# Kernel tuning notes

Measured on AMD Instinct MI355X. Metric: run time of the kernel, lower is better.

Reference implementation:

```python
import jax, jax.numpy as jnp
import numpy as np

EPS = 1e-6
NUM_SPECIAL = 4
NUM_HEADS = 16


def _rms_norm(x, w, eps=EPS):
    # x: [..., d], normalize over last dim
    var = jnp.mean(jnp.square(x), axis=-1, keepdims=True)
    return x * jax.lax.rsqrt(var + eps) * w


def _rotate_half(x):
    d = x.shape[-1] // 2
    return jnp.concatenate([-x[..., d:], x[..., :d]], axis=-1)


def _apply_rotary(q, k, cos, sin):
    # q,k: [B,H,N,hd]; cos,sin: [N,hd] -> broadcast [1,1,N,hd]
    cos = cos[None, None, :, :]
    sin = sin[None, None, :, :]
    q_out = q * cos + _rotate_half(q) * sin
    k_out = k * cos + _rotate_half(k) * sin
    return q_out, k_out


def _make_2d_mask(seq_len, num_special, window):
    # special tokens attend / are attended fully; patches use 2D local box
    patch_len = seq_len - num_special
    gs = int(round(patch_len ** 0.5))
    idx = jnp.arange(seq_len)
    special = idx < num_special
    p = idx - num_special
    row = p // gs
    col = p % gs
    special_case = special[:, None] | special[None, :]
    swa = (jnp.abs(row[:, None] - row[None, :]) <= window) & (
        jnp.abs(col[:, None] - col[None, :]) <= window)
    return special_case | swa  # [N, N] bool


def setup_inputs() -> dict:
    key = jax.random.key(0)
    ks = jax.random.split(key, 7)
    B, N, C = 4, 1028, 1024
    hd = C // NUM_HEADS
    return {
        "hidden_states": jax.random.normal(ks[0], (B, N, C), dtype=jnp.float32),
        "cos": jax.random.uniform(ks[1], (N, hd), dtype=jnp.float32),
        "sin": jax.random.uniform(ks[2], (N, hd), dtype=jnp.float32),
        "qkv_w": jax.random.normal(ks[3], (3 * C, C), dtype=jnp.float32) * (C ** -0.5),
        "out_w": jax.random.normal(ks[4], (C, C), dtype=jnp.float32) * (C ** -0.5),
        "norm_q_w": jnp.ones((hd,), dtype=jnp.float32),
        "norm_k_w": jnp.ones((hd,), dtype=jnp.float32),
        "sliding_window": 2,
    }


def reference(hidden_states, cos, sin, qkv_w, out_w, norm_q_w, norm_k_w, sliding_window):
    B, N, C = hidden_states.shape
    H = NUM_HEADS
    hd = C // H

    # fused QKV projection (nn.Linear: x @ W^T)
    qkv = jnp.einsum('bnc,dc->bnd', hidden_states, qkv_w)
    qkv = qkv.reshape(B, N, 3, H, hd).transpose(2, 0, 3, 1, 4)  # [3,B,H,N,hd]
    q, k, v = qkv[0], qkv[1], qkv[2]

    # per-head-dim RMSNorm on q and k
    q = _rms_norm(q, norm_q_w)
    k = _rms_norm(k, norm_k_w)

    # RoPE
    q, k = _apply_rotary(q, k, cos, sin)

    # 2D sliding-window + special-token mask
    mask = _make_2d_mask(N, NUM_SPECIAL, sliding_window)  # [N,N]

    scale = 1.0 / jnp.sqrt(jnp.asarray(hd, dtype=q.dtype))
    scores = jnp.einsum('bhqd,bhkd->bhqk', q, k) * scale
    neg = jnp.asarray(jnp.finfo(scores.dtype).min, dtype=scores.dtype)
    scores = jnp.where(mask[None, None, :, :], scores, neg)
    probs = jax.nn.softmax(scores, axis=-1)
    attn = jnp.einsum('bhqk,bhkd->bhqd', probs, v)  # [B,H,N,hd]

    attn = attn.transpose(0, 2, 1, 3).reshape(B, N, C)
    return jnp.einsum('bnc,dc->bnd', attn, out_w)
```

## Files before the change

kernel.cpp:

```cpp
#include <hip/hip_runtime.h>
#include <hip/hip_bf16.h>
#include <stdint.h>

typedef __bf16 bf16;
typedef __attribute__((ext_vector_type(8))) __bf16 bf16x8;
typedef __attribute__((ext_vector_type(4))) __bf16 bf16x4;
typedef __attribute__((ext_vector_type(4))) float f32x4;

#define NSEQ 1028
#define CDIM 1024
#define NHEADS 16
#define HD 64
#define BHN 64
#define NPAD 1088
#define M_REAL 4112
#define MTILES 33

static __device__ __forceinline__ void async_copy16(bf16* lds, const bf16* g) {
  __builtin_amdgcn_global_load_lds(
      (const __attribute__((address_space(1))) uint32_t*)g,
      (__attribute__((address_space(3))) uint32_t*)lds, 16, 0, 0);
}

__global__ __launch_bounds__(256) void cast3_kernel(
    const float* __restrict__ s0, bf16* __restrict__ d0, long n0,
    const float* __restrict__ s1, bf16* __restrict__ d1, long n1,
    const float* __restrict__ s2, bf16* __restrict__ d2, long n2) {
  long total = n0 + n1 + n2;
  long t = (long)blockIdx.x * 256 + threadIdx.x;
  long stride = (long)gridDim.x * 256;
  for (long j = t * 4; j < total; j += stride * 4) {
    const float* s; bf16* d; long jj = j;
    if (jj < n0) { s = s0; d = d0; }
    else if (jj < n0 + n1) { s = s1; d = d1; jj -= n0; }
    else { s = s2; d = d2; jj -= n0 + n1; }
    float4 v = *(const float4*)(s + jj);
    bf16x4 o;
    o[0] = (bf16)v.x; o[1] = (bf16)v.y; o[2] = (bf16)v.z; o[3] = (bf16)v.w;
    *(bf16x4*)(d + jj) = o;
  }
}

template <int EPI, int NSTRIP>
__global__ __launch_bounds__(256, 4) void gemm_bf16_kernel(
    const bf16* __restrict__ A, const bf16* __restrict__ Bm,
    bf16* __restrict__ q_bf, bf16* __restrict__ k_bf, bf16* __restrict__ v_raw,
    float* __restrict__ outF,
    const float* __restrict__ cosb, const float* __restrict__ sinb,
    const float* __restrict__ nqw, const float* __restrict__ nkw) {
  constexpr int K = CDIM;
  constexpr int N = NSTRIP * 8 * 128;
  __shared__ __attribute__((aligned(16))) bf16 As[2][128 * 32];
  __shared__ __attribute__((aligned(16))) bf16 Bs[2][128 * 32];
  const int tid = threadIdx.x;
  const int lane = tid & 63;
  const int wid = tid >> 6;
  const int wr = wid >> 1, wc = wid & 1;
  const int l15 = lane & 15, l4 = lane >> 4;

  const int xcd = blockIdx.x & 7;
  const int pos = blockIdx.x >> 3;
  const int nloc = pos % NSTRIP;
  const int mi = pos / NSTRIP;
  const int n0 = (xcd * NSTRIP + nloc) << 7;
  const int m0 = (mi < MTILES - 1) ? (mi << 7) : (M_REAL - 128);

  f32x4 acc[4][4] = {};

  size_t a_base[2], b_base[2];
#pragma unroll
  for (int s = 0; s < 2; s++) {
    int c = tid + s * 256;
    int u = c ^ ((c >> 3) & 7);
    int row = u >> 2, ch = u & 3;
    a_base[s] = (size_t)(m0 + row) * K + (ch << 3);
    b_base[s] = (size_t)(n0 + row) * K + (ch << 3);
  }

#define STAGE(bufi, ktof)                                         \
  {                                                               \
    _Pragma("unroll")                                             \
    for (int s = 0; s < 2; s++) {                                 \
      int c = tid + s * 256;                                      \
      async_copy16(&As[bufi][c * 8], A + a_base[s] + (ktof));     \
      async_copy16(&Bs[bufi][c * 8], Bm + b_base[s] + (ktof));    \
    }                                                             \
  }

  const int nt = K >> 5;
  STAGE(0, 0);

  for (int t = 0; t < nt; ++t) {
    if (t + 1 < nt) {
      STAGE((t + 1) & 1, (t + 1) << 5);
      asm volatile("s_waitcnt vmcnt(4)" ::: "memory");
    } else {
      asm volatile("s_waitcnt vmcnt(0)" ::: "memory");
    }
    __builtin_amdgcn_s_barrier();

    const int cur = t & 1;
    bf16x8 af[4], bfr[4];
#pragma unroll
    for (int i = 0; i < 4; i++) {
      int u = ((wr * 64 + i * 16 + l15) << 2) | l4;
      af[i] = *(const bf16x8*)&As[cur][(u ^ ((u >> 3) & 7)) << 3];
    }
#pragma unroll
    for (int j = 0; j < 4; j++) {
      int u = ((wc * 64 + j * 16 + l15) << 2) | l4;
      bfr[j] = *(const bf16x8*)&Bs[cur][(u ^ ((u >> 3) & 7)) << 3];
    }

#pragma unroll
    for (int i = 0; i < 4; i++)
#pragma unroll
      for (int j = 0; j < 4; j++)
        acc[i][j] = __builtin_amdgcn_mfma_f32_16x16x32_bf16(af[i], bfr[j], acc[i][j], 0, 0, 0);

    asm volatile("s_waitcnt lgkmcnt(0)" ::: "memory");
    __builtin_amdgcn_s_barrier();
  }
#undef STAGE

  if (EPI == 0) {
    const int d_base = n0 + wc * 64;
    const int tsel = d_base >> 10;
    const int hh = (d_base & 1023) >> 6;
    if (tsel == 2) {
#pragma unroll
      for (int i = 0; i < 4; i++)
#pragma unroll
        for (int r = 0; r < 4; r++) {
          int m = m0 + wr * 64 + i * 16 + l4 * 4 + r;
          int b = m / NSEQ, n = m % NSEQ;
          size_t rb = ((size_t)(b * NHEADS + hh) * NSEQ + n) * HD;
#pragma unroll
          for (int j = 0; j < 4; j++)
            v_raw[rb + j * 16 + l15] = (bf16)acc[i][j][r];
        }
    } else {
      const float* wn = (tsel == 0) ? nqw : nkw;
      bf16* dst = (tsel == 0) ? q_bf : k_bf;
      float wv[4];
#pragma unroll
      for (int j = 0; j < 4; j++) wv[j] = wn[j * 16 + l15];
#pragma unroll
      for (int i = 0; i < 4; i++)
#pragma unroll
        for (int r = 0; r < 4; r++) {
          int m = m0 + wr * 64 + i * 16 + l4 * 4 + r;
          float ss = 0.0f;
#pragma unroll
          for (int j = 0; j < 4; j++) { float x = acc[i][j][r]; ss += x * x; }
          ss += __shfl_xor(ss, 1);
          ss += __shfl_xor(ss, 2);
          ss += __shfl_xor(ss, 4);
          ss += __shfl_xor(ss, 8);
          float rms = rsqrtf(ss * (1.0f / HD) + 1e-6f);
          int b = m / NSEQ, n = m % NSEQ;
          float qn[4];
#pragma unroll
          for (int j = 0; j < 4; j++) qn[j] = acc[i][j][r] * rms * wv[j];
          size_t rb = ((size_t)(b * NHEADS + hh) * NPAD + n) * HD;
#pragma unroll
          for (int j = 0; j < 4; j++) {
            float c = cosb[n * HD + j * 16 + l15];
            float s = sinb[n * HD + j * 16 + l15];
            float rot = (j < 2) ? -qn[j + 2] : qn[j - 2];
            dst[rb + j * 16 + l15] = (bf16)(qn[j] * c + rot * s);
          }
        }
    }
  } else {
#pragma unroll
    for (int i = 0; i < 4; i++)
#pragma unroll
      for (int j = 0; j < 4; j++) {
        int d = n0 + wc * 64 + j * 16 + l15;
        int mrow = m0 + wr * 64 + i * 16 + l4 * 4;
#pragma unroll
        for (int r = 0; r < 4; r++) {
          int m = mrow + r;
          outF[(size_t)m * N + d] = acc[i][j][r];
        }
      }
  }
}

__global__ __launch_bounds__(256) void v_transpose_kernel(const bf16* __restrict__ v_raw,
                                                          bf16* __restrict__ vT) {
  __shared__ bf16 tile[64][65];
  int bh = blockIdx.y, c = blockIdx.x;
  int tid = threadIdx.x;
#pragma unroll
  for (int jj = 0; jj < 16; jj++) {
    int idx = tid + jj * 256;
    int i = idx >> 6, e = idx & 63;
    int n = (c == 0) ? i : (64 * c - 60 + i);
    bool ok = (c == 0) ? (i < 4) : (n < NSEQ);
    tile[i][e] = ok ? v_raw[((size_t)bh * NSEQ + n) * HD + e] : (bf16)0.0f;
  }
  __syncthreads();
#pragma unroll
  for (int jj = 0; jj < 16; jj++) {
    int idx = tid + jj * 256;
    int e = idx >> 6, i = idx & 63;
    vT[((size_t)bh * HD + e) * NPAD + 64 * c + i] = tile[i][e];
  }
}

__global__ __launch_bounds__(256) void attn_kernel(
    const bf16* __restrict__ Q, const bf16* __restrict__ Kb, const bf16* __restrict__ Vt,
    bf16* __restrict__ att, const int* __restrict__ winp) {
  __shared__ __attribute__((aligned(16))) bf16 P_s[4][16][72];
  __shared__ float o_s[4][4][64];
  __shared__ float ml_s[4][2][16];
  const int bh = blockIdx.y, qt = blockIdx.x;
  const int W = winp[0];
  const int tid = threadIdx.x, w = tid >> 6, lane = tid & 63;
  const int l15 = lane & 15, l4 = lane >> 4;
  const size_t qkbase = (size_t)bh * NPAD * HD;
  const size_t vtb = (size_t)bh * HD * NPAD;
  const bool is_spec = (qt == 16);

  const int qrow0 = is_spec ? 0 : (4 + qt * 64 + w * 16);
  bf16x8 aq0 = *(const bf16x8*)&Q[qkbase + (size_t)(qrow0 + l15) * HD + l4 * 8];
  bf16x8 aq1 = *(const bf16x8*)&Q[qkbase + (size_t)(qrow0 + l15) * HD + 32 + l4 * 8];

  float mrow[4], lrow[4];
  f32x4 o[4] = {};
#pragma unroll
  for (int r = 0; r < 4; r++) { mrow[r] = -1e30f; lrow[r] = 0.0f; }

  int p0, pstep, pmax, toff;
  if (is_spec) {
    p0 = w; pstep = 4; pmax = 16; toff = -1;
  } else {
    int ta = ((2 * qt - W + 64) >> 1) - 32;
    int tb = (2 * qt + 1 + W) >> 1;
    ta = ta < 0 ? 0 : ta;
    tb = tb > 15 ? 15 : tb;
    p0 = 0; pstep = 1; pmax = tb - ta + 1; toff = ta - 1;
  }

  for (int p = p0; p <= pmax; p += pstep) {
    const bool sp = (p == 0);
    const int tau = toff + p;
    const int krow0 = sp ? 0 : (4 + tau * 64);
    const int vcol0 = sp ? 0 : (64 + tau * 64);

    f32x4 sacc[4] = {};
#pragma unroll
    for (int kf = 0; kf < 4; kf++) {
      const bf16* kp = &Kb[qkbase + (size_t)(krow0 + kf * 16 + l15) * HD];
      bf16x8 b0 = *(const bf16x8*)(kp + l4 * 8);
      bf16x8 b1 = *(const bf16x8*)(kp + 32 + l4 * 8);
      sacc[kf] = __builtin_amdgcn_mfma_f32_16x16x32_bf16(aq0, b0, sacc[kf], 0, 0, 0);
      sacc[kf] = __builtin_amdgcn_mfma_f32_16x16x32_bf16(aq1, b1, sacc[kf], 0, 0, 0);
    }

    float pvv[4][4];
#pragma unroll
    for (int kf = 0; kf < 4; kf++)
#pragma unroll
      for (int r = 0; r < 4; r++) {
        float s = sacc[kf][r] * 0.125f;
        bool valid;
        if (sp) {
          valid = (kf == 0) && (l15 < 4);
        } else if (is_spec) {
          valid = true;
        } else {
          int p_k = tau * 64 + kf * 16 + l15;
          int p_q = qt * 64 + w * 16 + l4 * 4 + r;
          int dr = (p_q >> 5) - (p_k >> 5); dr = dr < 0 ? -dr : dr;
          int dc = (p_q & 31) - (p_k & 31); dc = dc < 0 ? -dc : dc;
          valid = (dr <= W) && (dc <= W);
        }
        pvv[kf][r] = valid ? s : -1e30f;
      }

#pragma unroll
    for (int r = 0; r < 4; r++) {
      float mx = fmaxf(fmaxf(pvv[0][r], pvv[1][r]), fmaxf(pvv[2][r], pvv[3][r]));
#pragma unroll
      for (int mm = 1; mm < 16; mm <<= 1) mx = fmaxf(mx, __shfl_xor(mx, mm));
      float mnew = fmaxf(mrow[r], mx);
      float scale = __expf(mrow[r] - mnew);
      float rs = 0.0f;
#pragma unroll
      for (int kf = 0; kf < 4; kf++) {
        float pp = __expf(pvv[kf][r] - mnew);
        pvv[kf][r] = pp;
        rs += pp;
      }
#pragma unroll
      for (int mm = 1; mm < 16; mm <<= 1) rs += __shfl_xor(rs, mm);
      lrow[r] = lrow[r] * scale + rs;
      mrow[r] = mnew;
#pragma unroll
      for (int f = 0; f < 4; f++) o[f][r] *= scale;
    }

#pragma unroll
    for (int kf = 0; kf < 4; kf++)
#pragma unroll
      for (int r = 0; r < 4; r++)
        P_s[w][l4 * 4 + r][kf * 16 + l15] = (bf16)pvv[kf][r];

    bf16x8 pa0 = *(const bf16x8*)&P_s[w][l15][l4 * 8];
    bf16x8 pa1 = *(const bf16x8*)&P_s[w][l15][32 + l4 * 8];
#pragma unroll
    for (int f = 0; f < 4; f++) {
      const bf16* vp = &Vt[vtb + (size_t)(f * 16 + l15) * NPAD + vcol0];
      bf16x8 v0 = *(const bf16x8*)(vp + l4 * 8);
      bf16x8 v1 = *(const bf16x8*)(vp + 32 + l4 * 8);
      o[f] = __builtin_amdgcn_mfma_f32_16x16x32_bf16(pa0, v0, o[f], 0, 0, 0);
      o[f] = __builtin_amdgcn_mfma_f32_16x16x32_bf16(pa1, v1, o[f], 0, 0, 0);
    }
  }

  const int b = bh >> 4, h = bh & 15;
  if (!is_spec) {
#pragma unroll
    for (int f = 0; f < 4; f++)
#pragma unroll
      for (int r = 0; r < 4; r++) {
        int n = qrow0 + l4 * 4 + r;
        att[((size_t)(b * NSEQ + n)) * CDIM + h * HD + f * 16 + l15] =
            (bf16)(o[f][r] / lrow[r]);
      }
  } else {
    if (l4 == 0) {
#pragma unroll
      for (int f = 0; f < 4; f++)
#pragma unroll
        for (int r = 0; r < 4; r++) o_s[w][r][f * 16 + l15] = o[f][r];
      if (l15 == 0)
#pragma unroll
        for (int r = 0; r < 4; r++) { ml_s[w][0][r] = mrow[r]; ml_s[w][1][r] = lrow[r]; }
    }
    __syncthreads();
    int row = tid >> 6, dim = tid & 63;
    float M = -1e30f;
#pragma unroll
    for (int ww = 0; ww < 4; ww++) M = fmaxf(M, ml_s[ww][0][row]);
    float L = 0.0f, val = 0.0f;
#pragma unroll
    for (int ww = 0; ww < 4; ww++) {
      float e = __expf(ml_s[ww][0][row] - M);
      L += e * ml_s[ww][1][row];
      val += e * o_s[ww][row][dim];
    }
    att[((size_t)(b * NSEQ + row)) * CDIM + h * HD + dim] = (bf16)(val / L);
  }
}

extern "C" void kernel_launch(void* const* d_in, const int* in_sizes, int n_in,
                              void* d_out, int out_size, void* d_ws, size_t ws_size,
                              hipStream_t stream) {
  const float* hidden = (const float*)d_in[0];
  const float* cosb = (const float*)d_in[1];
  const float* sinb = (const float*)d_in[2];
  const float* qkv_w = (const float*)d_in[3];
  const float* out_w = (const float*)d_in[4];
  const float* norm_q_w = (const float*)d_in[5];
  const float* norm_k_w = (const float*)d_in[6];
  const int* win = (const int*)d_in[7];
  float* out = (float*)d_out;

  char* ws = (char*)d_ws;
  size_t off = 0;
  auto alloc = [&](size_t bytes) {
    char* p = ws + off;
    off += (bytes + 255) & ~(size_t)255;
    return p;
  };
  bf16* A_bf  = (bf16*)alloc((size_t)M_REAL * CDIM * 2);
  bf16* W1    = (bf16*)alloc((size_t)3 * CDIM * CDIM * 2);
  bf16* W2    = (bf16*)alloc((size_t)CDIM * CDIM * 2);
  bf16* v_raw = (bf16*)alloc((size_t)BHN * NSEQ * HD * 2);
  bf16* q_bf  = (bf16*)alloc((size_t)BHN * NPAD * HD * 2);
  bf16* k_bf  = (bf16*)alloc((size_t)BHN * NPAD * HD * 2);
  bf16* vT    = (bf16*)alloc((size_t)BHN * HD * NPAD * 2);
  bf16* att   = (bf16*)alloc((size_t)M_REAL * CDIM * 2);
  (void)ws_size; (void)in_sizes; (void)n_in; (void)out_size;

  cast3_kernel<<<2048, 256, 0, stream>>>(
      hidden, A_bf, (long)M_REAL * CDIM,
      qkv_w, W1, (long)3 * CDIM * CDIM,
      out_w, W2, (long)CDIM * CDIM);

  gemm_bf16_kernel<0, 3><<<792, 256, 0, stream>>>(
      A_bf, W1, q_bf, k_bf, v_raw, nullptr, cosb, sinb, norm_q_w, norm_k_w);
  v_transpose_kernel<<<dim3(17, 64), 256, 0, stream>>>(v_raw, vT);
  attn_kernel<<<dim3(17, 64), 256, 0, stream>>>(q_bf, k_bf, vT, att, win);
  gemm_bf16_kernel<1, 1><<<264, 256, 0, stream>>>(
      att, W2, nullptr, nullptr, nullptr, out, nullptr, nullptr, nullptr, nullptr);
}
```

Before: 130.6 us.

## Load GEMM B operand directly to registers and shrink output GEMM N-tile

The GEMM no longer stages the weight (B) tile through LDS. Each wave reads its B fragments straight from global memory into registers every k-step, which halves the LDS footprint, and the occupancy hint rises from 4 to 6 blocks. The output projection now uses a 64-wide N tile with twice as many blocks, giving more parallelism. In exchange, the B loads are not prefetched, so global/L2 latency is exposed inside each k iteration, and weights are re-read per wave without LDS sharing.

```diff
diff --git a/kernel.cpp b/kernel.cpp
--- a/kernel.cpp
+++ b/kernel.cpp
@@ -41,17 +41,18 @@
   }
 }
 
-template <int EPI, int NSTRIP>
-__global__ __launch_bounds__(256, 4) void gemm_bf16_kernel(
+template <int EPI, int NSTRIP, int BN>
+__global__ __launch_bounds__(256, 6) void gemm_bf16_kernel(
     const bf16* __restrict__ A, const bf16* __restrict__ Bm,
     bf16* __restrict__ q_bf, bf16* __restrict__ k_bf, bf16* __restrict__ v_raw,
     float* __restrict__ outF,
     const float* __restrict__ cosb, const float* __restrict__ sinb,
     const float* __restrict__ nqw, const float* __restrict__ nkw) {
   constexpr int K = CDIM;
-  constexpr int N = NSTRIP * 8 * 128;
+  constexpr int N = NSTRIP * 8 * BN;
+  constexpr int HN = BN / 2;
+  constexpr int NJ = BN / 32;
   __shared__ __attribute__((aligned(16))) bf16 As[2][128 * 32];
-  __shared__ __attribute__((aligned(16))) bf16 Bs[2][128 * 32];
   const int tid = threadIdx.x;
   const int lane = tid & 63;
   const int wid = tid >> 6;
@@ -62,60 +63,58 @@
   const int pos = blockIdx.x >> 3;
   const int nloc = pos % NSTRIP;
   const int mi = pos / NSTRIP;
-  const int n0 = (xcd * NSTRIP + nloc) << 7;
+  const int n0 = (xcd * NSTRIP + nloc) * BN;
   const int m0 = (mi < MTILES - 1) ? (mi << 7) : (M_REAL - 128);
 
-  f32x4 acc[4][4] = {};
-
-  size_t a_base[2], b_base[2];
+  f32x4 acc[4][NJ] = {};
+
+  size_t a_base[2];
 #pragma unroll
   for (int s = 0; s < 2; s++) {
     int c = tid + s * 256;
     int u = c ^ ((c >> 3) & 7);
-    int row = u >> 2, ch = u & 3;
-    a_base[s] = (size_t)(m0 + row) * K + (ch << 3);
-    b_base[s] = (size_t)(n0 + row) * K + (ch << 3);
-  }
+    a_base[s] = (size_t)(m0 + (u >> 2)) * K + ((u & 3) << 3);
+  }
+
+  const size_t b_uni = (size_t)(n0 + wc * HN) * K;
+  const int b_lane = l15 * K + l4 * 8;
 
 #define STAGE(bufi, ktof)                                         \
   {                                                               \
     _Pragma("unroll")                                             \
-    for (int s = 0; s < 2; s++) {                                 \
-      int c = tid + s * 256;                                      \
-      async_copy16(&As[bufi][c * 8], A + a_base[s] + (ktof));     \
-      async_copy16(&Bs[bufi][c * 8], Bm + b_base[s] + (ktof));    \
-    }                                                             \
+    for (int s = 0; s < 2; s++)                                   \
+      async_copy16(&As[bufi][(tid + s * 256) * 8], A + a_base[s] + (ktof)); \
   }
 
   const int nt = K >> 5;
   STAGE(0, 0);
 
   for (int t = 0; t < nt; ++t) {
+    bf16x8 bfr[NJ];
+#pragma unroll
+    for (int j = 0; j < NJ; j++)
+      bfr[j] = *(const bf16x8*)(Bm + b_uni + (size_t)j * 16 * K + b_lane + (t << 5));
+
     if (t + 1 < nt) {
       STAGE((t + 1) & 1, (t + 1) << 5);
-      asm volatile("s_waitcnt vmcnt(4)" ::: "memory");
+      asm volatile("s_waitcnt vmcnt(2)" ::: "memory");
     } else {
       asm volatile("s_waitcnt vmcnt(0)" ::: "memory");
     }
     __builtin_amdgcn_s_barrier();
 
     const int cur = t & 1;
-    bf16x8 af[4], bfr[4];
+    bf16x8 af[4];
 #pragma unroll
     for (int i = 0; i < 4; i++) {
       int u = ((wr * 64 + i * 16 + l15) << 2) | l4;
       af[i] = *(const bf16x8*)&As[cur][(u ^ ((u >> 3) & 7)) << 3];
     }
-#pragma unroll
-    for (int j = 0; j < 4; j++) {
-      int u = ((wc * 64 + j * 16 + l15) << 2) | l4;
-      bfr[j] = *(const bf16x8*)&Bs[cur][(u ^ ((u >> 3) & 7)) << 3];
-    }
 
 #pragma unroll
     for (int i = 0; i < 4; i++)
 #pragma unroll
-      for (int j = 0; j < 4; j++)
+      for (int j = 0; j < NJ; j++)
         acc[i][j] = __builtin_amdgcn_mfma_f32_16x16x32_bf16(af[i], bfr[j], acc[i][j], 0, 0, 0);
 
     asm volatile("s_waitcnt lgkmcnt(0)" ::: "memory");
@@ -136,15 +135,15 @@
           int b = m / NSEQ, n = m % NSEQ;
           size_t rb = ((size_t)(b * NHEADS + hh) * NSEQ + n) * HD;
 #pragma unroll
-          for (int j = 0; j < 4; j++)
+          for (int j = 0; j < NJ; j++)
             v_raw[rb + j * 16 + l15] = (bf16)acc[i][j][r];
         }
     } else {
       const float* wn = (tsel == 0) ? nqw : nkw;
       bf16* dst = (tsel == 0) ? q_bf : k_bf;
-      float wv[4];
-#pragma unroll
-      for (int j = 0; j < 4; j++) wv[j] = wn[j * 16 + l15];
+      float wv[NJ];
+#pragma unroll
+      for (int j = 0; j < NJ; j++) wv[j] = wn[j * 16 + l15];
 #pragma unroll
       for (int i = 0; i < 4; i++)
 #pragma unroll
@@ -152,19 +151,19 @@
           int m = m0 + wr * 64 + i * 16 + l4 * 4 + r;
           float ss = 0.0f;
 #pragma unroll
-          for (int j = 0; j < 4; j++) { float x = acc[i][j][r]; ss += x * x; }
+          for (int j = 0; j < NJ; j++) { float x = acc[i][j][r]; ss += x * x; }
           ss += __shfl_xor(ss, 1);
           ss += __shfl_xor(ss, 2);
           ss += __shfl_xor(ss, 4);
           ss += __shfl_xor(ss, 8);
           float rms = rsqrtf(ss * (1.0f / HD) + 1e-6f);
           int b = m / NSEQ, n = m % NSEQ;
-          float qn[4];
-#pragma unroll
-          for (int j = 0; j < 4; j++) qn[j] = acc[i][j][r] * rms * wv[j];
+          float qn[NJ];
+#pragma unroll
+          for (int j = 0; j < NJ; j++) qn[j] = acc[i][j][r] * rms * wv[j];
           size_t rb = ((size_t)(b * NHEADS + hh) * NPAD + n) * HD;
 #pragma unroll
-          for (int j = 0; j < 4; j++) {
+          for (int j = 0; j < NJ; j++) {
             float c = cosb[n * HD + j * 16 + l15];
             float s = sinb[n * HD + j * 16 + l15];
             float rot = (j < 2) ? -qn[j + 2] : qn[j - 2];
@@ -176,8 +175,8 @@
 #pragma unroll
     for (int i = 0; i < 4; i++)
 #pragma unroll
-      for (int j = 0; j < 4; j++) {
-        int d = n0 + wc * 64 + j * 16 + l15;
+      for (int j = 0; j < NJ; j++) {
+        int d = n0 + wc * HN + j * 16 + l15;
         int mrow = m0 + wr * 64 + i * 16 + l4 * 4;
 #pragma unroll
         for (int r = 0; r < 4; r++) {
@@ -392,10 +391,10 @@
       qkv_w, W1, (long)3 * CDIM * CDIM,
       out_w, W2, (long)CDIM * CDIM);
 
-  gemm_bf16_kernel<0, 3><<<792, 256, 0, stream>>>(
+  gemm_bf16_kernel<0, 3, 128><<<792, 256, 0, stream>>>(
       A_bf, W1, q_bf, k_bf, v_raw, nullptr, cosb, sinb, norm_q_w, norm_k_w);
   v_transpose_kernel<<<dim3(17, 64), 256, 0, stream>>>(v_raw, vT);
   attn_kernel<<<dim3(17, 64), 256, 0, stream>>>(q_bf, k_bf, vT, att, win);
-  gemm_bf16_kernel<1, 1><<<264, 256, 0, stream>>>(
+  gemm_bf16_kernel<1, 2, 64><<<528, 256, 0, stream>>>(
       att, W2, nullptr, nullptr, nullptr, out, nullptr, nullptr, nullptr, nullptr);
 }
```

Measured after the change: 328.1 us. +151.2%, slower.

## Split output projection GEMM into intra-block split-K with 64-wide tiles

Applied to the files above, without the earlier changes.

The output projection now uses a dedicated kernel with 128x64 tiles and 528 blocks instead of 264 128x128 blocks. Inside each block, two wave pairs each handle half of K and reduce their partial sums through LDS before the fp32 store. This is meant to fill the GPU's compute units better, since the old launch had too few blocks. It also adds s_setprio around MFMA sections in the GEMM and attention kernels to favour matrix issue. The cost is extra LDS traffic for the reduction and more loads per output.

```diff
diff --git a/kernel.cpp b/kernel.cpp
--- a/kernel.cpp
+++ b/kernel.cpp
@@ -41,15 +41,13 @@
   }
 }
 
-template <int EPI, int NSTRIP>
-__global__ __launch_bounds__(256, 4) void gemm_bf16_kernel(
+__global__ __launch_bounds__(256, 4) void gemm_qkv_kernel(
     const bf16* __restrict__ A, const bf16* __restrict__ Bm,
     bf16* __restrict__ q_bf, bf16* __restrict__ k_bf, bf16* __restrict__ v_raw,
-    float* __restrict__ outF,
     const float* __restrict__ cosb, const float* __restrict__ sinb,
     const float* __restrict__ nqw, const float* __restrict__ nkw) {
   constexpr int K = CDIM;
-  constexpr int N = NSTRIP * 8 * 128;
+  constexpr int NSTRIP = 3;
   __shared__ __attribute__((aligned(16))) bf16 As[2][128 * 32];
   __shared__ __attribute__((aligned(16))) bf16 Bs[2][128 * 32];
   const int tid = threadIdx.x;
@@ -72,19 +70,17 @@
   for (int s = 0; s < 2; s++) {
     int c = tid + s * 256;
     int u = c ^ ((c >> 3) & 7);
-    int row = u >> 2, ch = u & 3;
-    a_base[s] = (size_t)(m0 + row) * K + (ch << 3);
-    b_base[s] = (size_t)(n0 + row) * K + (ch << 3);
-  }
-
-#define STAGE(bufi, ktof)                                         \
-  {                                                               \
-    _Pragma("unroll")                                             \
-    for (int s = 0; s < 2; s++) {                                 \
-      int c = tid + s * 256;                                      \
-      async_copy16(&As[bufi][c * 8], A + a_base[s] + (ktof));     \
-      async_copy16(&Bs[bufi][c * 8], Bm + b_base[s] + (ktof));    \
-    }                                                             \
+    a_base[s] = (size_t)(m0 + (u >> 2)) * K + ((u & 3) << 3);
+    b_base[s] = (size_t)(n0 + (u >> 2)) * K + ((u & 3) << 3);
+  }
+
+#define STAGE(bufi, ktof)                                                   \
+  {                                                                         \
+    _Pragma("unroll")                                                       \
+    for (int s = 0; s < 2; s++) {                                           \
+      async_copy16(&As[bufi][(tid + s * 256) * 8], A + a_base[s] + (ktof)); \
+      async_copy16(&Bs[bufi][(tid + s * 256) * 8], Bm + b_base[s] + (ktof));\
+    }                                                                       \
   }
 
   const int nt = K >> 5;
@@ -123,68 +119,174 @@
   }
 #undef STAGE
 
-  if (EPI == 0) {
-    const int d_base = n0 + wc * 64;
-    const int tsel = d_base >> 10;
-    const int hh = (d_base & 1023) >> 6;
-    if (tsel == 2) {
-#pragma unroll
-      for (int i = 0; i < 4; i++)
-#pragma unroll
-        for (int r = 0; r < 4; r++) {
-          int m = m0 + wr * 64 + i * 16 + l4 * 4 + r;
-          int b = m / NSEQ, n = m % NSEQ;
-          size_t rb = ((size_t)(b * NHEADS + hh) * NSEQ + n) * HD;
-#pragma unroll
-          for (int j = 0; j < 4; j++)
-            v_raw[rb + j * 16 + l15] = (bf16)acc[i][j][r];
-        }
-    } else {
-      const float* wn = (tsel == 0) ? nqw : nkw;
-      bf16* dst = (tsel == 0) ? q_bf : k_bf;
-      float wv[4];
-#pragma unroll
-      for (int j = 0; j < 4; j++) wv[j] = wn[j * 16 + l15];
-#pragma unroll
-      for (int i = 0; i < 4; i++)
-#pragma unroll
-        for (int r = 0; r < 4; r++) {
-          int m = m0 + wr * 64 + i * 16 + l4 * 4 + r;
-          float ss = 0.0f;
-#pragma unroll
-          for (int j = 0; j < 4; j++) { float x = acc[i][j][r]; ss += x * x; }
-          ss += __shfl_xor(ss, 1);
-          ss += __shfl_xor(ss, 2);
-          ss += __shfl_xor(ss, 4);
-          ss += __shfl_xor(ss, 8);
-          float rms = rsqrtf(ss * (1.0f / HD) + 1e-6f);
-          int b = m / NSEQ, n = m % NSEQ;
-          float qn[4];
-#pragma unroll
-          for (int j = 0; j < 4; j++) qn[j] = acc[i][j][r] * rms * wv[j];
-          size_t rb = ((size_t)(b * NHEADS + hh) * NPAD + n) * HD;
-#pragma unroll
-          for (int j = 0; j < 4; j++) {
-            float c = cosb[n * HD + j * 16 + l15];
-            float s = sinb[n * HD + j * 16 + l15];
-            float rot = (j < 2) ? -qn[j + 2] : qn[j - 2];
-            dst[rb + j * 16 + l15] = (bf16)(qn[j] * c + rot * s);
-          }
-        }
-    }
+  const int d_base = n0 + wc * 64;
+  const int tsel = d_base >> 10;
+  const int hh = (d_base & 1023) >> 6;
+  if (tsel == 2) {
+#pragma unroll
+    for (int i = 0; i < 4; i++)
+#pragma unroll
+      for (int r = 0; r < 4; r++) {
+        int m = m0 + wr * 64 + i * 16 + l4 * 4 + r;
+        int b = m / NSEQ, n = m % NSEQ;
+        size_t rb = ((size_t)(b * NHEADS + hh) * NSEQ + n) * HD;
+#pragma unroll
+        for (int j = 0; j < 4; j++)
+          v_raw[rb + j * 16 + l15] = (bf16)acc[i][j][r];
+      }
   } else {
+    const float* wn = (tsel == 0) ? nqw : nkw;
+    bf16* dst = (tsel == 0) ? q_bf : k_bf;
+    float wv[4];
+#pragma unroll
+    for (int j = 0; j < 4; j++) wv[j] = wn[j * 16 + l15];
 #pragma unroll
     for (int i = 0; i < 4; i++)
 #pragma unroll
-      for (int j = 0; j < 4; j++) {
-        int d = n0 + wc * 64 + j * 16 + l15;
-        int mrow = m0 + wr * 64 + i * 16 + l4 * 4;
-#pragma unroll
-        for (int r = 0; r < 4; r++) {
-          int m = mrow + r;
-          outF[(size_t)m * N + d] = acc[i][j][r];
+      for (int r = 0; r < 4; r++) {
+        int m = m0 + wr * 64 + i * 16 + l4 * 4 + r;
+        float ss = 0.0f;
+#pragma unroll
+        for (int j = 0; j < 4; j++) { float x = acc[i][j][r]; ss += x * x; }
+        ss += __shfl_xor(ss, 1);
+        ss += __shfl_xor(ss, 2);
+        ss += __shfl_xor(ss, 4);
+        ss += __shfl_xor(ss, 8);
+        float rms = rsqrtf(ss * (1.0f / HD) + 1e-6f);
+        int b = m / NSEQ, n = m % NSEQ;
+        float qn[4];
+#pragma unroll
+        for (int j = 0; j < 4; j++) qn[j] = acc[i][j][r] * rms * wv[j];
+        size_t rb = ((size_t)(b * NHEADS + hh) * NPAD + n) * HD;
+#pragma unroll
+        for (int j = 0; j < 4; j++) {
+          float c = cosb[n * HD + j * 16 + l15];
+          float s = sinb[n * HD + j * 16 + l15];
+          float rot = (j < 2) ? -qn[j + 2] : qn[j - 2];
+          dst[rb + j * 16 + l15] = (bf16)(qn[j] * c + rot * s);
         }
       }
+  }
+}
+
+__global__ __launch_bounds__(256, 3) void gemm2_splitk_kernel(
+    const bf16* __restrict__ A, const bf16* __restrict__ Bm,
+    float* __restrict__ outF) {
+  constexpr int K = CDIM;
+  constexpr int KH = 512;
+  constexpr int N = CDIM;
+  __shared__ __attribute__((aligned(16))) bf16 As[2][2][128 * 32];
+  __shared__ __attribute__((aligned(16))) bf16 Bs[2][2][64 * 32];
+  const int tid = threadIdx.x;
+  const int lane = tid & 63;
+  const int wid = tid >> 6;
+  const int mh = wid & 1;
+  const int kh = wid >> 1;
+  const int l15 = lane & 15, l4 = lane >> 4;
+
+  const int xcd = blockIdx.x & 7;
+  const int pos = blockIdx.x >> 3;
+  const int nloc = pos % 2;
+  const int mi = pos / 2;
+  const int n0 = (xcd * 2 + nloc) * 64;
+  const int m0 = (mi < MTILES - 1) ? (mi << 7) : (M_REAL - 128);
+
+  f32x4 acc[4][4] = {};
+
+  size_t a_src[4]; int a_off[4];
+#pragma unroll
+  for (int s = 0; s < 4; s++) {
+    int c = tid + s * 256;
+    int half = c >> 9, u = c & 511;
+    int uu = u ^ ((u >> 3) & 7);
+    a_src[s] = (size_t)(m0 + (uu >> 2)) * K + half * KH + ((uu & 3) << 3);
+    a_off[s] = half * 4096 + u * 8;
+  }
+  size_t b_src[2]; int b_off[2];
+#pragma unroll
+  for (int s = 0; s < 2; s++) {
+    int c = tid + s * 256;
+    int half = c >> 8, u = c & 255;
+    int uu = u ^ ((u >> 3) & 7);
+    b_src[s] = (size_t)(n0 + (uu >> 2)) * K + half * KH + ((uu & 3) << 3);
+    b_off[s] = half * 2048 + u * 8;
+  }
+  bf16* as_flat = (bf16*)As;
+  bf16* bs_flat = (bf16*)Bs;
+
+#define STAGE2(bufi, ktof)                                                  \
+  {                                                                         \
+    _Pragma("unroll")                                                       \
+    for (int s = 0; s < 4; s++)                                             \
+      async_copy16(as_flat + (bufi) * 8192 + a_off[s], A + a_src[s] + (ktof)); \
+    _Pragma("unroll")                                                       \
+    for (int s = 0; s < 2; s++)                                             \
+      async_copy16(bs_flat + (bufi) * 4096 + b_off[s], Bm + b_src[s] + (ktof)); \
+  }
+
+  const int nt = KH >> 5;
+  STAGE2(0, 0);
+
+  for (int t = 0; t < nt; ++t) {
+    if (t + 1 < nt) {
+      STAGE2((t + 1) & 1, (t + 1) << 5);
+      asm volatile("s_waitcnt vmcnt(6)" ::: "memory");
+    } else {
+      asm volatile("s_waitcnt vmcnt(0)" ::: "memory");
+    }
+    __builtin_amdgcn_s_barrier();
+
+    const int cur = t & 1;
+    bf16x8 af[4], bfr[4];
+#pragma unroll
+    for (int i = 0; i < 4; i++) {
+      int u = ((mh * 64 + i * 16 + l15) << 2) | l4;
+      af[i] = *(const bf16x8*)(as_flat + cur * 8192 + kh * 4096 +
+                               ((u ^ ((u >> 3) & 7)) << 3));
+    }
+#pragma unroll
+    for (int j = 0; j < 4; j++) {
+      int u = ((j * 16 + l15) << 2) | l4;
+      bfr[j] = *(const bf16x8*)(bs_flat + cur * 4096 + kh * 2048 +
+                                ((u ^ ((u >> 3) & 7)) << 3));
+    }
+
+    __builtin_amdgcn_s_setprio(1);
+#pragma unroll
+    for (int i = 0; i < 4; i++)
+#pragma unroll
+      for (int j = 0; j < 4; j++)
+        acc[i][j] = __builtin_amdgcn_mfma_f32_16x16x32_bf16(af[i], bfr[j], acc[i][j], 0, 0, 0);
+    __builtin_amdgcn_s_setprio(0);
+
+    asm volatile("s_waitcnt lgkmcnt(0)" ::: "memory");
+    __builtin_amdgcn_s_barrier();
+  }
+#undef STAGE2
+
+  float* red = (float*)As;
+  if (kh == 1) {
+#pragma unroll
+    for (int i = 0; i < 4; i++)
+#pragma unroll
+      for (int j = 0; j < 4; j++)
+#pragma unroll
+        for (int r = 0; r < 4; r++)
+          red[mh * 4096 + (i * 16 + l4 * 4 + r) * 64 + j * 16 + l15] = acc[i][j][r];
+  }
+  __syncthreads();
+  if (kh == 0) {
+#pragma unroll
+    for (int i = 0; i < 4; i++)
+#pragma unroll
+      for (int j = 0; j < 4; j++)
+#pragma unroll
+        for (int r = 0; r < 4; r++) {
+          float v = acc[i][j][r] +
+                    red[mh * 4096 + (i * 16 + l4 * 4 + r) * 64 + j * 16 + l15];
+          int m = m0 + mh * 64 + i * 16 + l4 * 4 + r;
+          outF[(size_t)m * N + n0 + j * 16 + l15] = v;
+        }
   }
 }
 
@@ -251,6 +353,7 @@
     const int vcol0 = sp ? 0 : (64 + tau * 64);
 
     f32x4 sacc[4] = {};
+    __builtin_amdgcn_s_setprio(1);
 #pragma unroll
     for (int kf = 0; kf < 4; kf++) {
       const bf16* kp = &Kb[qkbase + (size_t)(krow0 + kf * 16 + l15) * HD];
@@ -259,6 +362,7 @@
       sacc[kf] = __builtin_amdgcn_mfma_f32_16x16x32_bf16(aq0, b0, sacc[kf], 0, 0, 0);
       sacc[kf] = __builtin_amdgcn_mfma_f32_16x16x32_bf16(aq1, b1, sacc[kf], 0, 0, 0);
     }
+    __builtin_amdgcn_s_setprio(0);
 
     float pvv[4][4];
 #pragma unroll
@@ -311,6 +415,7 @@
 
     bf16x8 pa0 = *(const bf16x8*)&P_s[w][l15][l4 * 8];
     bf16x8 pa1 = *(const bf16x8*)&P_s[w][l15][32 + l4 * 8];
+    __builtin_amdgcn_s_setprio(1);
 #pragma unroll
     for (int f = 0; f < 4; f++) {
       const bf16* vp = &Vt[vtb + (size_t)(f * 16 + l15) * NPAD + vcol0];
@@ -319,6 +424,7 @@
       o[f] = __builtin_amdgcn_mfma_f32_16x16x32_bf16(pa0, v0, o[f], 0, 0, 0);
       o[f] = __builtin_amdgcn_mfma_f32_16x16x32_bf16(pa1, v1, o[f], 0, 0, 0);
     }
+    __builtin_amdgcn_s_setprio(0);
   }
 
   const int b = bh >> 4, h = bh & 15;
@@ -392,10 +498,9 @@
       qkv_w, W1, (long)3 * CDIM * CDIM,
       out_w, W2, (long)CDIM * CDIM);
 
-  gemm_bf16_kernel<0, 3><<<792, 256, 0, stream>>>(
-      A_bf, W1, q_bf, k_bf, v_raw, nullptr, cosb, sinb, norm_q_w, norm_k_w);
+  gemm_qkv_kernel<<<792, 256, 0, stream>>>(
+      A_bf, W1, q_bf, k_bf, v_raw, cosb, sinb, norm_q_w, norm_k_w);
   v_transpose_kernel<<<dim3(17, 64), 256, 0, stream>>>(v_raw, vT);
   attn_kernel<<<dim3(17, 64), 256, 0, stream>>>(q_bf, k_bf, vT, att, win);
-  gemm_bf16_kernel<1, 1><<<264, 256, 0, stream>>>(
-      att, W2, nullptr, nullptr, nullptr, out, nullptr, nullptr, nullptr, nullptr);
-}
+  gemm2_splitk_kernel<<<528, 256, 0, stream>>>(att, W2, out);
+}
```

New measurement: 134.7 us. 1.03x slower.
